# Optimization experiments

Measured on AMD Instinct MI355X. Metric: run time of the kernel, lower is better.

## Reference

```python
import math
import jax, jax.numpy as jnp
import numpy as np

B, N, L, E, H, T = 64, 8, 128, 768, 12, 64


def setup_inputs() -> dict:
    key = jax.random.key(0)
    ks = jax.random.split(key, 8)
    s = 0.02
    return {
        "x":  jax.random.normal(ks[0], (B, N, L, E), dtype=jnp.float32),
        # torch Linear weights are [out, in]
        "Wq": jax.random.normal(ks[1], (H, E, E), dtype=jnp.float32) * s,
        "bq": jax.random.normal(ks[2], (H, E), dtype=jnp.float32) * s,
        "Wv": jax.random.normal(ks[3], (H, T, E), dtype=jnp.float32) * s,
        "bv": jax.random.normal(ks[4], (H, T), dtype=jnp.float32) * s,
        "Wf": jax.random.normal(ks[5], (E, H * T), dtype=jnp.float32) * s,
        "bf": jax.random.normal(ks[6], (E,), dtype=jnp.float32) * s,
    }


def reference(x, Wq, bq, Wv, bv, Wf, bf):
    b, n, l, e = x.shape
    S = b * n                      # set_size after the view(-1, L, E)
    x2 = x.reshape(S, l, e)
    # per-head query projection (batched over heads)
    Q = jnp.einsum('sle,hfe->hslf', x2, Wq) + bq[:, None, None, :]      # [H,S,L,E]
    # raw (unsoftmaxed) attention: (Q K^T) V / sqrt(E)
    scores = jnp.einsum('hslf,smf->hslm', Q, x2)                        # [H,S,L,L]
    attn = jnp.einsum('hslm,sme->hsle', scores, x2) * (1.0 / math.sqrt(e))
    # per-head value projection to transformer_dim
    V = jnp.einsum('hsle,hte->hslt', attn, Wv) + bv[:, None, None, :]   # [H,S,L,T]
    # concat heads along last dim (head order preserved)
    cat = jnp.transpose(V, (1, 2, 0, 3)).reshape(S, l, -1)              # [S,L,H*T]
    out = cat @ Wf.T + bf                                               # [S,L,E]
    return out.reshape(b, n, l, e)
```

## Files before the change

### kernel.cpp

```cpp
#include <hip/hip_runtime.h>
#include <stdint.h>


#define EE 768
#define SLOT 50331648L

typedef short s16x8 __attribute__((ext_vector_type(8)));
typedef float f32x4 __attribute__((ext_vector_type(4)));

__device__ __forceinline__ short f2bf(float f){
  union { float fv; uint32_t u; } v; v.fv = f;
  uint32_t r = (v.u + 0x7fffu + ((v.u >> 16) & 1u)) >> 16;
  return (short)r;
}

__device__ __forceinline__ void gld_lds16(const short* g, short* l){
  __builtin_amdgcn_global_load_lds(
      (const __attribute__((address_space(1))) void*)(uintptr_t)g,
      (__attribute__((address_space(3))) void*)(uintptr_t)l,
      16, 0, 0);
}

__device__ __forceinline__ int xcd_swz(int bid, int nwg){
  int xcd = bid & 7, loc = bid >> 3;
  int q = nwg >> 3, r = nwg & 7;
  return (xcd < r ? xcd * (q + 1) : r * (q + 1) + (xcd - r) * q) + loc;
}

__device__ __forceinline__ int swz64(int row, int c){ return c ^ ((row & 7) << 3); }
__device__ __forceinline__ int swz32(int row, int c){ return c ^ (((row >> 1) & 3) << 3); }

__global__ __launch_bounds__(256) void cast_bf16_k(const float* __restrict__ src,
                                                   short* __restrict__ dst,
                                                   long n, float scale){
  long i = ((long)blockIdx.x * 256 + threadIdx.x) * 8;
  if(i >= n) return;
  float4 a = *(const float4*)(src + i);
  float4 b = *(const float4*)(src + i + 4);
  s16x8 o;
  o[0]=f2bf(a.x*scale); o[1]=f2bf(a.y*scale); o[2]=f2bf(a.z*scale); o[3]=f2bf(a.w*scale);
  o[4]=f2bf(b.x*scale); o[5]=f2bf(b.y*scale); o[6]=f2bf(b.z*scale); o[7]=f2bf(b.w*scale);
  *(s16x8*)(dst + i) = o;
}

__global__ __launch_bounds__(256) void cvec_k(const float* __restrict__ Wf,
                                              const float* __restrict__ bv,
                                              const float* __restrict__ bfv,
                                              float* __restrict__ c){
  int e = blockIdx.x * 256 + threadIdx.x;
  if(e >= EE) return;
  float s = bfv[e];
  for(int k = 0; k < EE; ++k) s += Wf[(long)e * EE + k] * bv[k];
  c[e] = s;
}

__global__ __launch_bounds__(256) void bias_build(const float* __restrict__ bq,
                                                  float* __restrict__ biasQP){
  int i = blockIdx.x * 256 + threadIdx.x;
  if(i < 9984) biasQP[i] = (i < 9216) ? bq[i] : 0.f;
}

template<bool OUTF32>
__global__ __launch_bounds__(512, 1) void gemm8ph(const short* __restrict__ A,
                                                  const short* __restrict__ W,
                                                  const float* __restrict__ bias,
                                                  void* __restrict__ OutBase,
                                                  int hBase, int nSub, int pSub){
  extern __shared__ short lds[];
  const int tid = threadIdx.x, lane = tid & 63, w = tid >> 6;
  const int wr = w >> 2, wc = w & 3;
  const int bid = xcd_swz(blockIdx.x, nSub * 768);
  const int g = bid / 768, rb = bid - g * 768;
  const int rowBlk = rb / 3, colBlk = rb - rowBlk * 3;
  const long rowA0 = (long)rowBlk * 256;
  const int colB0 = colBlk * 256;
  const int wh = (g == pSub) ? 12 : hBase + g;
  const short* Bm = W + (long)wh * 589824L;

  const int slr = w * 16 + (lane >> 2);
  const int scol = swz32(slr, (lane & 3) * 8);
  const short* gA0 = A + (rowA0 + slr) * 768 + scol;
  const short* gA1 = A + (rowA0 + 128 + slr) * 768 + scol;
  const short* gB0 = Bm + (long)(colB0 + slr) * 768 + scol;
  const short* gB1 = Bm + (long)(colB0 + 128 + slr) * 768 + scol;

  auto stageA = [&](int kt){
    short* Al = lds + (kt & 3) * 16384;
    gld_lds16(gA0 + kt * 32, Al + (w * 16) * 32);
    gld_lds16(gA1 + kt * 32, Al + (128 + w * 16) * 32);
  };
  auto stageB = [&](int kt){
    short* Bl = lds + (kt & 3) * 16384 + 8192;
    gld_lds16(gB0 + kt * 32, Bl + (w * 16) * 32);
    gld_lds16(gB1 + kt * 32, Bl + (128 + w * 16) * 32);
  };

  f32x4 acc[8][4] = {};
  const int fr = lane & 15, fc = (lane >> 4) * 8;

  stageA(0); stageB(0); stageA(1); stageB(1); stageA(2); stageB(2);
  asm volatile("s_waitcnt vmcnt(8)\n\ts_barrier" ::: "memory");

  for(int t = 0; t < 24; ++t){
    const short* Al = lds + (t & 3) * 16384;
    const short* Bl = Al + 8192;
    s16x8 bfr[4], af[4];
    #pragma unroll
    for(int n = 0; n < 4; ++n){
      int row = wc * 64 + n * 16 + fr;
      bfr[n] = *(const s16x8*)&Bl[row * 32 + swz32(row, fc)];
    }
    #pragma unroll
    for(int m = 0; m < 4; ++m){
      int row = wr * 128 + m * 16 + fr;
      af[m] = *(const s16x8*)&Al[row * 32 + swz32(row, fc)];
    }
    if(t < 21) stageA(t + 3);
    asm volatile("s_barrier" ::: "memory");
    __builtin_amdgcn_s_setprio(1);
    #pragma unroll
    for(int m = 0; m < 4; ++m)
      #pragma unroll
      for(int n = 0; n < 4; ++n)
        acc[m][n] = __builtin_amdgcn_mfma_f32_16x16x32_bf16(af[m], bfr[n], acc[m][n], 0, 0, 0);
    __builtin_amdgcn_s_setprio(0);
    asm volatile("s_barrier" ::: "memory");
    #pragma unroll
    for(int m = 0; m < 4; ++m){
      int row = wr * 128 + 64 + m * 16 + fr;
      af[m] = *(const s16x8*)&Al[row * 32 + swz32(row, fc)];
    }
    if(t < 21) stageB(t + 3);
    if(t < 21)       asm volatile("s_waitcnt vmcnt(8)" ::: "memory");
    else if(t == 21) asm volatile("s_waitcnt vmcnt(4)" ::: "memory");
    else             asm volatile("s_waitcnt vmcnt(0)" ::: "memory");
    asm volatile("s_barrier" ::: "memory");
    __builtin_amdgcn_s_setprio(1);
    #pragma unroll
    for(int m = 0; m < 4; ++m)
      #pragma unroll
      for(int n = 0; n < 4; ++n)
        acc[4 + m][n] = __builtin_amdgcn_mfma_f32_16x16x32_bf16(af[m], bfr[n], acc[4 + m][n], 0, 0, 0);
    __builtin_amdgcn_s_setprio(0);
    asm volatile("s_barrier" ::: "memory");
  }

  asm volatile("s_waitcnt vmcnt(0) lgkmcnt(0)" ::: "memory");
  __syncthreads();

  float bb[4];
  #pragma unroll
  for(int n = 0; n < 4; ++n)
    bb[n] = bias[wh * 768 + colB0 + wc * 64 + n * 16 + fr];

  if constexpr(!OUTF32){
    short* Out = (short*)OutBase + (long)g * SLOT;
    short* Cs = lds;
    #pragma unroll
    for(int ch = 0; ch < 2; ++ch){
      __syncthreads();
      if(wr == ch){
        #pragma unroll
        for(int m = 0; m < 8; ++m)
          #pragma unroll
          for(int n = 0; n < 4; ++n)
            #pragma unroll
            for(int r2 = 0; r2 < 4; ++r2){
              int row = m * 16 + (lane >> 4) * 4 + r2;
              int c = wc * 64 + n * 16 + fr;
              Cs[row * 256 + (c ^ (((row >> 2) & 3) << 4))] = f2bf(acc[m][n][r2] + bb[n]);
            }
      }
      __syncthreads();
      #pragma unroll
      for(int i = 0; i < 8; ++i){
        int idx = i * 512 + tid;
        int row = idx >> 5, cl = (idx & 31) * 8;
        s16x8 v = *(const s16x8*)&Cs[row * 256 + (cl ^ (((row >> 2) & 3) << 4))];
        *(s16x8*)&Out[(rowA0 + ch * 128 + row) * 768 + colB0 + cl] = v;
      }
    }
  } else {
    float* Co = (float*)OutBase;
    const long crow0 = rowA0 + wr * 128;
    #pragma unroll
    for(int mf = 0; mf < 8; ++mf)
      #pragma unroll
      for(int n = 0; n < 4; ++n)
        #pragma unroll
        for(int r2 = 0; r2 < 4; ++r2){
          const long row = crow0 + mf * 16 + (lane >> 4) * 4 + r2;
          const int col = colB0 + wc * 64 + n * 16 + fr;
          Co[row * 768 + col] = acc[mf][n][r2] + bb[n];
        }
  }
}

__global__ __launch_bounds__(512, 1) void gemm256(const short* __restrict__ A,
                                                  const short* __restrict__ W,
                                                  const float* __restrict__ bias,
                                                  short* __restrict__ OutBase,
                                                  int hBase, int nSub, int pSub){
  __shared__ short lds[2][16384];
  const int tid = threadIdx.x, lane = tid & 63, w = tid >> 6;
  const int wr = w >> 2, wc = w & 3;
  const int bid = xcd_swz(blockIdx.x, nSub * 768);
  const int g = bid / 768, rb = bid - g * 768;
  const int rowBlk = rb / 3, colBlk = rb - rowBlk * 3;
  const long rowA0 = (long)rowBlk * 256;
  const int colB0 = colBlk * 256;
  const int wh = (g == pSub) ? 12 : hBase + g;
  const short* Bm = W + (long)wh * 589824L;
  short* Out = OutBase + (long)g * SLOT;

  const int sr0 = w * 32 + (lane >> 2);
  const int sr1 = sr0 + 16;
  const int scol = (lane & 3) * 8;
  const int sc0 = swz32(sr0, scol);
  const int sc1 = swz32(sr1, scol);
  const short* Ar0 = A + (rowA0 + sr0) * 768;
  const short* Ar1 = A + (rowA0 + sr1) * 768;
  const short* Br0 = Bm + (long)(colB0 + sr0) * 768;
  const short* Br1 = Bm + (long)(colB0 + sr1) * 768;

  f32x4 acc[8][4] = {};
  s16x8 af[4], bf0[2], bf1[2];
  const int fr = lane & 15, fc = (lane >> 4) * 8;

  auto stage = [&](int b, int kt){
    short* Al = &lds[b][0];
    short* Bl = &lds[b][8192];
    gld_lds16(Ar0 + kt + sc0, Al + (w * 2) * 512);
    gld_lds16(Ar1 + kt + sc1, Al + (w * 2 + 1) * 512);
    gld_lds16(Br0 + kt + sc0, Bl + (w * 2) * 512);
    gld_lds16(Br1 + kt + sc1, Bl + (w * 2 + 1) * 512);
  };

  stage(0, 0);
  for(int t = 0; t < 24; ++t){
    if(t < 23){
      stage((t + 1) & 1, (t + 1) * 32);
      asm volatile("s_waitcnt vmcnt(4)\n\ts_barrier" ::: "memory");
    } else {
      asm volatile("s_waitcnt vmcnt(0)\n\ts_barrier" ::: "memory");
    }
    const short* Al = &lds[t & 1][0];
    const short* Bl = &lds[t & 1][8192];

    auto loadA = [&](int mh){
      #pragma unroll
      for(int m = 0; m < 4; ++m){
        int row = wr * 128 + (mh * 4 + m) * 16 + fr;
        af[m] = *(const s16x8*)&Al[row * 32 + swz32(row, fc)];
      }
    };
    auto loadB = [&](int nh, s16x8* bf){
      #pragma unroll
      for(int n = 0; n < 2; ++n){
        int row = wc * 64 + (nh * 2 + n) * 16 + fr;
        bf[n] = *(const s16x8*)&Bl[row * 32 + swz32(row, fc)];
      }
    };
    auto mm = [&](int mh, int nh, s16x8* bf){
      __builtin_amdgcn_s_setprio(1);
      #pragma unroll
      for(int m = 0; m < 4; ++m)
        #pragma unroll
        for(int n = 0; n < 2; ++n)
          acc[mh * 4 + m][nh * 2 + n] = __builtin_amdgcn_mfma_f32_16x16x32_bf16(
              af[m], bf[n], acc[mh * 4 + m][nh * 2 + n], 0, 0, 0);
      __builtin_amdgcn_s_setprio(0);
    };

    loadA(0); loadB(0, bf0); mm(0, 0, bf0);
    loadB(1, bf1);           mm(0, 1, bf1);
    loadA(1);                mm(1, 1, bf1);
    loadB(0, bf0);           mm(1, 0, bf0);
    asm volatile("s_barrier" ::: "memory");
  }

  float bb[4];
  #pragma unroll
  for(int n = 0; n < 4; ++n)
    bb[n] = bias[wh * 768 + colB0 + wc * 64 + n * 16 + fr];

  short* Cs = &lds[0][0];
  #pragma unroll
  for(int ch = 0; ch < 2; ++ch){
    __syncthreads();
    if(wr == ch){
      #pragma unroll
      for(int m = 0; m < 8; ++m)
        #pragma unroll
        for(int n = 0; n < 4; ++n)
          #pragma unroll
          for(int r2 = 0; r2 < 4; ++r2){
            int row = m * 16 + (lane >> 4) * 4 + r2;
            int c = wc * 64 + n * 16 + fr;
            Cs[row * 256 + (c ^ (((row >> 2) & 3) << 4))] = f2bf(acc[m][n][r2] + bb[n]);
          }
    }
    __syncthreads();
    #pragma unroll
    for(int i = 0; i < 8; ++i){
      int idx = i * 512 + tid;
      int row = idx >> 5, cl = (idx & 31) * 8;
      s16x8 v = *(const s16x8*)&Cs[row * 256 + (cl ^ (((row >> 2) & 3) << 4))];
      *(s16x8*)&Out[(rowA0 + ch * 128 + row) * 768 + colB0 + cl] = v;
    }
  }
}

__global__ __launch_bounds__(256, 2) void gemm_f32(const short* __restrict__ A,
                                                   const short* __restrict__ B,
                                                   const float* __restrict__ bias,
                                                   float* __restrict__ Cout){
  __shared__ short smem[4 * 8192];
  const int tid = threadIdx.x, lane = tid & 63, w = tid >> 6;
  const int wr = w >> 1, wc = w & 1;
  const int nCol = 6;
  const int xcd = blockIdx.x & 7, loc = blockIdx.x >> 3;
  const int width = nCol << 3;
  const int gid = loc / width, rem = loc % width;
  const int rowBlk = (xcd << 6) + (gid << 3) + (rem & 7);
  const int colBlk = rem >> 3;
  const long rowA0 = (long)rowBlk << 7;
  const long colB0 = (long)colBlk << 7;
  const int lr = lane >> 3;
  const int sA = swz64(lr, (lane & 7) * 8);

  f32x4 acc[4][4] = {};
  auto stage = [&](int b, int kt){
    short* As = smem + b * 16384;
    #pragma unroll
    for(int it = 0; it < 4; ++it){
      int r = it * 32 + w * 8;
      gld_lds16(&A[(rowA0 + r + lr) * 768 + kt + sA], &As[r * 64]);
      gld_lds16(&B[(colB0 + r + lr) * 768 + kt + sA], &As[8192 + r * 64]);
    }
  };

  stage(0, 0);
  for(int t = 0; t < 12; ++t){
    const int cur = t & 1;
    if(t < 11){
      stage(cur ^ 1, (t + 1) * 64);
      asm volatile("s_waitcnt vmcnt(8)\n\ts_barrier" ::: "memory");
    } else {
      asm volatile("s_waitcnt vmcnt(0)\n\ts_barrier" ::: "memory");
    }
    const short* As = smem + cur * 16384;
    const short* Bs = As + 8192;
    #pragma unroll
    for(int kk = 0; kk < 2; ++kk){
      s16x8 af[4], bfr[4];
      #pragma unroll
      for(int m = 0; m < 4; ++m){
        int row = wr * 64 + m * 16 + (lane & 15);
        af[m] = *(const s16x8*)&As[row * 64 + swz64(row, kk * 32 + (lane >> 4) * 8)];
      }
      #pragma unroll
      for(int n = 0; n < 4; ++n){
        int row = wc * 64 + n * 16 + (lane & 15);
        bfr[n] = *(const s16x8*)&Bs[row * 64 + swz64(row, kk * 32 + (lane >> 4) * 8)];
      }
      #pragma unroll
      for(int m = 0; m < 4; ++m)
        #pragma unroll
        for(int n = 0; n < 4; ++n)
          acc[m][n] = __builtin_amdgcn_mfma_f32_16x16x32_bf16(af[m], bfr[n], acc[m][n], 0, 0, 0);
    }
    asm volatile("s_barrier" ::: "memory");
  }

  const long crow0 = rowA0 + wr * 64;
  const long ccol0 = colB0 + wc * 64;
  #pragma unroll
  for(int n = 0; n < 4; ++n){
    const long col = ccol0 + n * 16 + (lane & 15);
    const float bbv = bias[col];
    #pragma unroll
    for(int m = 0; m < 4; ++m)
      #pragma unroll
      for(int r = 0; r < 4; ++r){
        const long row = crow0 + m * 16 + (lane >> 4) * 4 + r;
        Cout[row * 768 + col] = acc[m][n][r] + bbv;
      }
  }
}

__global__ __launch_bounds__(256, 2) void attn_k(const short* __restrict__ Q,
                                                 const short* __restrict__ P,
                                                 const short* __restrict__ X,
                                                 short* __restrict__ Cat,
                                                 int h0, int nH){
  __shared__ short smem[4 * 8192];
  const int tid = threadIdx.x, lane = tid & 63, w = tid >> 6;
  const int wr = w >> 1, wc = w & 1;
  const int nwg = nH << 9;
  const int bid = xcd_swz(blockIdx.x, nwg);
  const int s = bid / nH, hi = bid - s * nH, h = h0 + hi;
  const long row0 = (long)s * 128;
  const int lr = lane >> 3;
  const int sA = swz64(lr, (lane & 7) * 8);

  const int pm = tid >> 3, pt0 = (tid & 7) * 8;
  s16x8 pv[4];
  #pragma unroll
  for(int i = 0; i < 4; ++i)
    pv[i] = *(const s16x8*)&P[(row0 + pm + i * 32) * 768L + h * 64 + pt0];

  f32x4 acc[4][4] = {};
  const short* Qh = Q + (long)hi * SLOT;
  auto stage = [&](int b, int kt){
    short* As = smem + b * 16384;
    #pragma unroll
    for(int it = 0; it < 4; ++it){
      int r = it * 32 + w * 8;
      gld_lds16(&Qh[(row0 + r + lr) * 768L + kt + sA], &As[r * 64]);
      gld_lds16(&X[(row0 + r + lr) * 768L + kt + sA], &As[8192 + r * 64]);
    }
  };

  stage(0, 0);
  for(int t = 0; t < 12; ++t){
    const int cur = t & 1;
    if(t < 11){
      stage(cur ^ 1, (t + 1) * 64);
      asm volatile("s_waitcnt vmcnt(8)\n\ts_barrier" ::: "memory");
    } else {
      asm volatile("s_waitcnt vmcnt(0)\n\ts_barrier" ::: "memory");
    }
    const short* As = smem + cur * 16384;
    const short* Bs = As + 8192;
    #pragma unroll
    for(int kk = 0; kk < 2; ++kk){
      s16x8 af[4], bfr[4];
      #pragma unroll
      for(int m = 0; m < 4; ++m){
        int row = wr * 64 + m * 16 + (lane & 15);
        af[m] = *(const s16x8*)&As[row * 64 + swz64(row, kk * 32 + (lane >> 4) * 8)];
      }
      #pragma unroll
      for(int n = 0; n < 4; ++n){
        int row = wc * 64 + n * 16 + (lane & 15);
        bfr[n] = *(const s16x8*)&Bs[row * 64 + swz64(row, kk * 32 + (lane >> 4) * 8)];
      }
      #pragma unroll
      for(int m = 0; m < 4; ++m)
        #pragma unroll
        for(int n = 0; n < 4; ++n)
          acc[m][n] = __builtin_amdgcn_mfma_f32_16x16x32_bf16(af[m], bfr[n], acc[m][n], 0, 0, 0);
    }
    asm volatile("s_barrier" ::: "memory");
  }

  short* Pt = smem;
  short* Vt = smem + 8192;
  short* Ss = smem + 16384;

  #pragma unroll
  for(int m = 0; m < 4; ++m)
    #pragma unroll
    for(int n = 0; n < 4; ++n)
      #pragma unroll
      for(int r = 0; r < 4; ++r){
        int row = wr * 64 + m * 16 + (lane >> 4) * 4 + r;
        int c = wc * 64 + n * 16 + (lane & 15);
        Ss[row * 128 + swz64(row, c)] = f2bf(acc[m][n][r]);
      }
  #pragma unroll
  for(int i = 0; i < 4; ++i)
    #pragma unroll
    for(int j = 0; j < 8; ++j){
      int trow = pt0 + j;
      int mc = pm + i * 32;
      Pt[trow * 128 + swz64(trow, mc)] = pv[i][j];
    }
  __syncthreads();

  f32x4 accv[2][4] = {};
  #pragma unroll
  for(int kk = 0; kk < 4; ++kk){
    s16x8 a2[2], b4[4];
    #pragma unroll
    for(int m = 0; m < 2; ++m){
      int row = w * 32 + m * 16 + (lane & 15);
      a2[m] = *(const s16x8*)&Ss[row * 128 + swz64(row, kk * 32 + (lane >> 4) * 8)];
    }
    #pragma unroll
    for(int n = 0; n < 4; ++n){
      int trow = n * 16 + (lane & 15);
      b4[n] = *(const s16x8*)&Pt[trow * 128 + swz64(trow, kk * 32 + (lane >> 4) * 8)];
    }
    #pragma unroll
    for(int m = 0; m < 2; ++m)
      #pragma unroll
      for(int n = 0; n < 4; ++n)
        accv[m][n] = __builtin_amdgcn_mfma_f32_16x16x32_bf16(a2[m], b4[n], accv[m][n], 0, 0, 0);
  }

  #pragma unroll
  for(int m = 0; m < 2; ++m)
    #pragma unroll
    for(int n = 0; n < 4; ++n)
      #pragma unroll
      for(int r = 0; r < 4; ++r){
        int row = w * 32 + m * 16 + (lane >> 4) * 4 + r;
        int c = n * 16 + (lane & 15);
        Vt[row * 64 + swz64(row, c)] = f2bf(accv[m][n][r]);
      }
  __syncthreads();
  #pragma unroll
  for(int k2 = 0; k2 < 4; ++k2){
    int row = k2 * 32 + (tid >> 3);
    int cl = (tid & 7) * 8;
    s16x8 v = *(const s16x8*)&Vt[row * 64 + swz64(row, cl)];
    *(s16x8*)&Cat[(row0 + row) * 768L + h * 64 + cl] = v;
  }
}

extern "C" void kernel_launch(void* const* d_in, const int* in_sizes, int n_in,
                              void* d_out, int out_size, void* d_ws, size_t ws_size,
                              hipStream_t stream){
  const float* x  = (const float*)d_in[0];
  const float* Wq = (const float*)d_in[1];
  const float* bq = (const float*)d_in[2];
  const float* Wv = (const float*)d_in[3];
  const float* bv = (const float*)d_in[4];
  const float* Wf = (const float*)d_in[5];
  const float* bfv= (const float*)d_in[6];

  const float rsqE = 0.03608439182435161f;
  char* ws = (char*)d_ws;

  short* Xb  = (short*)(ws);
  short* Cat = (short*)(ws + 100663296L);
  short* Wb  = (short*)(ws + 201326592L);
  short* Wfb = (short*)(ws + 216662016L);
  float* bQP = (float*)(ws + 217841664L);
  float* cv  = (float*)(ws + 217881600L);
  short* QS  = (short*)(ws + 217884672L);

  const size_t QOFF = 217884672ULL;
  int G = 1;
  const int cands[5] = {12, 6, 4, 3, 2};
  for(int i = 0; i < 5; ++i)
    if(ws_size >= QOFF + (size_t)(cands[i] + 1) * 100663296ULL){ G = cands[i]; break; }
  short* Pall = QS + (long)G * SLOT;

  bool deep =
      hipFuncSetAttribute(reinterpret_cast<const void*>(&gemm8ph<false>),
                          hipFuncAttributeMaxDynamicSharedMemorySize, 131072) == hipSuccess &&
      hipFuncSetAttribute(reinterpret_cast<const void*>(&gemm8ph<true>),
                          hipFuncAttributeMaxDynamicSharedMemorySize, 131072) == hipSuccess;

  dim3 b256(256), b512(512);
  cast_bf16_k<<<24576, b256, 0, stream>>>(x,  Xb, 50331648L, 1.f);
  cast_bf16_k<<<3456,  b256, 0, stream>>>(Wq, Wb, 7077888L, 1.f);
  cast_bf16_k<<<288,   b256, 0, stream>>>(Wv, Wb + 7077888L, 589824L, rsqE);
  cast_bf16_k<<<288,   b256, 0, stream>>>(Wf, Wfb, 589824L, 1.f);
  bias_build<<<39, b256, 0, stream>>>(bq, bQP);
  cvec_k<<<3, b256, 0, stream>>>(Wf, bv, bfv, cv);

  const int nB = 12 / G;
  for(int b = 0; b < nB; ++b){
    const int nSub = G + (b == 0 ? 1 : 0);
    const int pSub = (b == 0) ? G : -1;
    if(deep)
      gemm8ph<false><<<dim3(nSub * 768), b512, 131072, stream>>>(Xb, Wb, bQP, QS, b * G, nSub, pSub);
    else
      gemm256<<<dim3(nSub * 768), b512, 0, stream>>>(Xb, Wb, bQP, QS, b * G, nSub, pSub);
    attn_k<<<dim3(G * 512), b256, 0, stream>>>(QS, Pall, Xb, Cat, b * G, G);
  }
  if(deep)
    gemm8ph<true><<<dim3(768), b512, 131072, stream>>>(Cat, Wfb, cv, d_out, 0, 1, -1);
  else
    gemm_f32<<<dim3(3072), b256, 0, stream>>>(Cat, Wfb, cv, (float*)d_out);
}
```

Measured before the change: 1.765 ms.

## Rewrite GEMM main loop with register double-buffered fragments and fused staging

The projection GEMM's main loop drops the eight-phase schedule, which split the A fragments into two halves with four barriers per k-step. Each k-step now issues one combined A+B async load into the LDS ring and takes a single barrier. Fragments for the next k-tile are read into a second register set while MFMAs run on the current one. This cuts barrier count and lets LDS reads overlap with matrix math, at the cost of more VGPRs and a possible write-after-read race on the LDS ring, since slots are refilled without a barrier after the last read.

```diff
diff --git a/kernel.cpp b/kernel.cpp
--- a/kernel.cpp
+++ b/kernel.cpp
@@ -61,7 +61,7 @@
 }
 
 template<bool OUTF32>
-__global__ __launch_bounds__(512, 1) void gemm8ph(const short* __restrict__ A,
+__global__ __launch_bounds__(512, 1) void gemm_rb(const short* __restrict__ A,
                                                   const short* __restrict__ W,
                                                   const float* __restrict__ bias,
                                                   void* __restrict__ OutBase,
@@ -84,66 +84,74 @@
   const short* gB0 = Bm + (long)(colB0 + slr) * 768 + scol;
   const short* gB1 = Bm + (long)(colB0 + 128 + slr) * 768 + scol;
 
-  auto stageA = [&](int kt){
+  auto stageK = [&](int kt){
     short* Al = lds + (kt & 3) * 16384;
     gld_lds16(gA0 + kt * 32, Al + (w * 16) * 32);
     gld_lds16(gA1 + kt * 32, Al + (128 + w * 16) * 32);
-  };
-  auto stageB = [&](int kt){
-    short* Bl = lds + (kt & 3) * 16384 + 8192;
-    gld_lds16(gB0 + kt * 32, Bl + (w * 16) * 32);
-    gld_lds16(gB1 + kt * 32, Bl + (128 + w * 16) * 32);
+    gld_lds16(gB0 + kt * 32, Al + 8192 + (w * 16) * 32);
+    gld_lds16(gB1 + kt * 32, Al + 8192 + (128 + w * 16) * 32);
   };
 
   f32x4 acc[8][4] = {};
   const int fr = lane & 15, fc = (lane >> 4) * 8;
 
-  stageA(0); stageB(0); stageA(1); stageB(1); stageA(2); stageB(2);
-  asm volatile("s_waitcnt vmcnt(8)\n\ts_barrier" ::: "memory");
-
-  for(int t = 0; t < 24; ++t){
+  s16x8 A0[8], B0[4], A1[8], B1[4];
+
+  auto readF = [&](int t, s16x8* Af, s16x8* Bf){
     const short* Al = lds + (t & 3) * 16384;
     const short* Bl = Al + 8192;
-    s16x8 bfr[4], af[4];
+    #pragma unroll
+    for(int m = 0; m < 8; ++m){
+      int row = wr * 128 + m * 16 + fr;
+      Af[m] = *(const s16x8*)&Al[row * 32 + swz32(row, fc)];
+    }
     #pragma unroll
     for(int n = 0; n < 4; ++n){
       int row = wc * 64 + n * 16 + fr;
-      bfr[n] = *(const s16x8*)&Bl[row * 32 + swz32(row, fc)];
-    }
-    #pragma unroll
-    for(int m = 0; m < 4; ++m){
-      int row = wr * 128 + m * 16 + fr;
-      af[m] = *(const s16x8*)&Al[row * 32 + swz32(row, fc)];
-    }
-    if(t < 21) stageA(t + 3);
-    asm volatile("s_barrier" ::: "memory");
+      Bf[n] = *(const s16x8*)&Bl[row * 32 + swz32(row, fc)];
+    }
+  };
+  auto mfmaC = [&](s16x8* Af, s16x8* Bf){
     __builtin_amdgcn_s_setprio(1);
     #pragma unroll
-    for(int m = 0; m < 4; ++m)
+    for(int m = 0; m < 8; ++m)
       #pragma unroll
       for(int n = 0; n < 4; ++n)
-        acc[m][n] = __builtin_amdgcn_mfma_f32_16x16x32_bf16(af[m], bfr[n], acc[m][n], 0, 0, 0);
+        acc[m][n] = __builtin_amdgcn_mfma_f32_16x16x32_bf16(Af[m], Bf[n], acc[m][n], 0, 0, 0);
     __builtin_amdgcn_s_setprio(0);
-    asm volatile("s_barrier" ::: "memory");
-    #pragma unroll
-    for(int m = 0; m < 4; ++m){
-      int row = wr * 128 + 64 + m * 16 + fr;
-      af[m] = *(const s16x8*)&Al[row * 32 + swz32(row, fc)];
-    }
-    if(t < 21) stageB(t + 3);
-    if(t < 21)       asm volatile("s_waitcnt vmcnt(8)" ::: "memory");
-    else if(t == 21) asm volatile("s_waitcnt vmcnt(4)" ::: "memory");
-    else             asm volatile("s_waitcnt vmcnt(0)" ::: "memory");
-    asm volatile("s_barrier" ::: "memory");
-    __builtin_amdgcn_s_setprio(1);
-    #pragma unroll
-    for(int m = 0; m < 4; ++m)
-      #pragma unroll
-      for(int n = 0; n < 4; ++n)
-        acc[4 + m][n] = __builtin_amdgcn_mfma_f32_16x16x32_bf16(af[m], bfr[n], acc[4 + m][n], 0, 0, 0);
-    __builtin_amdgcn_s_setprio(0);
-    asm volatile("s_barrier" ::: "memory");
-  }
+  };
+
+  stageK(0); stageK(1); stageK(2);
+  asm volatile("s_waitcnt vmcnt(8)" ::: "memory");
+  __builtin_amdgcn_s_barrier();
+  readF(0, A0, B0);
+
+  for(int tt = 0; tt < 20; tt += 2){
+    stageK(tt + 3);
+    asm volatile("s_waitcnt vmcnt(8)" ::: "memory");
+    __builtin_amdgcn_s_barrier();
+    readF(tt + 1, A1, B1);
+    mfmaC(A0, B0);
+    stageK(tt + 4);
+    asm volatile("s_waitcnt vmcnt(8)" ::: "memory");
+    __builtin_amdgcn_s_barrier();
+    readF(tt + 2, A0, B0);
+    mfmaC(A1, B1);
+  }
+  stageK(23);
+  asm volatile("s_waitcnt vmcnt(8)" ::: "memory");
+  __builtin_amdgcn_s_barrier();
+  readF(21, A1, B1);
+  mfmaC(A0, B0);
+  asm volatile("s_waitcnt vmcnt(4)" ::: "memory");
+  __builtin_amdgcn_s_barrier();
+  readF(22, A0, B0);
+  mfmaC(A1, B1);
+  asm volatile("s_waitcnt vmcnt(0)" ::: "memory");
+  __builtin_amdgcn_s_barrier();
+  readF(23, A1, B1);
+  mfmaC(A0, B0);
+  mfmaC(A1, B1);
 
   asm volatile("s_waitcnt vmcnt(0) lgkmcnt(0)" ::: "memory");
   __syncthreads();
@@ -550,9 +558,9 @@
   short* Pall = QS + (long)G * SLOT;
 
   bool deep =
-      hipFuncSetAttribute(reinterpret_cast<const void*>(&gemm8ph<false>),
+      hipFuncSetAttribute(reinterpret_cast<const void*>(&gemm_rb<false>),
                           hipFuncAttributeMaxDynamicSharedMemorySize, 131072) == hipSuccess &&
-      hipFuncSetAttribute(reinterpret_cast<const void*>(&gemm8ph<true>),
+      hipFuncSetAttribute(reinterpret_cast<const void*>(&gemm_rb<true>),
                           hipFuncAttributeMaxDynamicSharedMemorySize, 131072) == hipSuccess;
 
   dim3 b256(256), b512(512);
@@ -568,13 +576,13 @@
     const int nSub = G + (b == 0 ? 1 : 0);
     const int pSub = (b == 0) ? G : -1;
     if(deep)
-      gemm8ph<false><<<dim3(nSub * 768), b512, 131072, stream>>>(Xb, Wb, bQP, QS, b * G, nSub, pSub);
+      gemm_rb<false><<<dim3(nSub * 768), b512, 131072, stream>>>(Xb, Wb, bQP, QS, b * G, nSub, pSub);
     else
       gemm256<<<dim3(nSub * 768), b512, 0, stream>>>(Xb, Wb, bQP, QS, b * G, nSub, pSub);
     attn_k<<<dim3(G * 512), b256, 0, stream>>>(QS, Pall, Xb, Cat, b * G, G);
   }
   if(deep)
-    gemm8ph<true><<<dim3(768), b512, 131072, stream>>>(Cat, Wfb, cv, d_out, 0, 1, -1);
+    gemm_rb<true><<<dim3(768), b512, 131072, stream>>>(Cat, Wfb, cv, d_out, 0, 1, -1);
   else
     gemm_f32<<<dim3(3072), b256, 0, stream>>>(Cat, Wfb, cv, (float*)d_out);
 }
```

Result: no change. 1.769 ms (+0.2%).

## Switch GEMM to 32x32x16 MFMA tiles with unified A/B staging

Applied to the files above, without the earlier changes.

Replaces the 16x16x32 bf16 MFMA tiling in the main GEMM kernel with 32x32x16 MFMAs, which gives each wave 4x2 accumulator tiles and halves the LDS fragment reads per FLOP. A and B stages for each k-tile are now issued together instead of being split across two phases, and both k-halves are read from LDS up front. The epilogue index mapping is rewritten for the 32x32 accumulator layout. Risks include a different LDS bank-conflict pattern under the existing swizzle, higher register pressure, and changed overlap of loads with compute.

```diff
diff --git a/kernel.cpp b/kernel.cpp
--- a/kernel.cpp
+++ b/kernel.cpp
@@ -7,6 +7,7 @@
 
 typedef short s16x8 __attribute__((ext_vector_type(8)));
 typedef float f32x4 __attribute__((ext_vector_type(4)));
+typedef float f32x16 __attribute__((ext_vector_type(16)));
 
 __device__ __forceinline__ short f2bf(float f){
   union { float fv; uint32_t u; } v; v.fv = f;
@@ -61,11 +62,11 @@
 }
 
 template<bool OUTF32>
-__global__ __launch_bounds__(512, 1) void gemm8ph(const short* __restrict__ A,
-                                                  const short* __restrict__ W,
-                                                  const float* __restrict__ bias,
-                                                  void* __restrict__ OutBase,
-                                                  int hBase, int nSub, int pSub){
+__global__ __launch_bounds__(512, 1) void gemm32(const short* __restrict__ A,
+                                                 const short* __restrict__ W,
+                                                 const float* __restrict__ bias,
+                                                 void* __restrict__ OutBase,
+                                                 int hBase, int nSub, int pSub){
   extern __shared__ short lds[];
   const int tid = threadIdx.x, lane = tid & 63, w = tid >> 6;
   const int wr = w >> 2, wc = w & 3;
@@ -84,74 +85,70 @@
   const short* gB0 = Bm + (long)(colB0 + slr) * 768 + scol;
   const short* gB1 = Bm + (long)(colB0 + 128 + slr) * 768 + scol;
 
-  auto stageA = [&](int kt){
+  auto stageK = [&](int kt){
     short* Al = lds + (kt & 3) * 16384;
     gld_lds16(gA0 + kt * 32, Al + (w * 16) * 32);
     gld_lds16(gA1 + kt * 32, Al + (128 + w * 16) * 32);
+    gld_lds16(gB0 + kt * 32, Al + 8192 + (w * 16) * 32);
+    gld_lds16(gB1 + kt * 32, Al + 8192 + (128 + w * 16) * 32);
   };
-  auto stageB = [&](int kt){
-    short* Bl = lds + (kt & 3) * 16384 + 8192;
-    gld_lds16(gB0 + kt * 32, Bl + (w * 16) * 32);
-    gld_lds16(gB1 + kt * 32, Bl + (128 + w * 16) * 32);
-  };
-
-  f32x4 acc[8][4] = {};
-  const int fr = lane & 15, fc = (lane >> 4) * 8;
-
-  stageA(0); stageB(0); stageA(1); stageB(1); stageA(2); stageB(2);
-  asm volatile("s_waitcnt vmcnt(8)\n\ts_barrier" ::: "memory");
-
-  for(int t = 0; t < 24; ++t){
+
+  f32x16 acc[4][2] = {};
+  const int lrow = lane & 31;
+  const int kh = (lane >> 5) * 8;
+
+  auto readAB = [&](int t, int kk, s16x8* Af, s16x8* Bf){
     const short* Al = lds + (t & 3) * 16384;
     const short* Bl = Al + 8192;
-    s16x8 bfr[4], af[4];
-    #pragma unroll
-    for(int n = 0; n < 4; ++n){
-      int row = wc * 64 + n * 16 + fr;
-      bfr[n] = *(const s16x8*)&Bl[row * 32 + swz32(row, fc)];
-    }
-    #pragma unroll
-    for(int m = 0; m < 4; ++m){
-      int row = wr * 128 + m * 16 + fr;
-      af[m] = *(const s16x8*)&Al[row * 32 + swz32(row, fc)];
-    }
-    if(t < 21) stageA(t + 3);
-    asm volatile("s_barrier" ::: "memory");
+    const int colv = kk * 16 + kh;
+    #pragma unroll
+    for(int rt = 0; rt < 4; ++rt){
+      int row = wr * 128 + rt * 32 + lrow;
+      Af[rt] = *(const s16x8*)&Al[row * 32 + swz32(row, colv)];
+    }
+    #pragma unroll
+    for(int ct = 0; ct < 2; ++ct){
+      int row = wc * 64 + ct * 32 + lrow;
+      Bf[ct] = *(const s16x8*)&Bl[row * 32 + swz32(row, colv)];
+    }
+  };
+  auto mm8 = [&](s16x8* Af, s16x8* Bf){
     __builtin_amdgcn_s_setprio(1);
     #pragma unroll
-    for(int m = 0; m < 4; ++m)
-      #pragma unroll
-      for(int n = 0; n < 4; ++n)
-        acc[m][n] = __builtin_amdgcn_mfma_f32_16x16x32_bf16(af[m], bfr[n], acc[m][n], 0, 0, 0);
+    for(int rt = 0; rt < 4; ++rt)
+      #pragma unroll
+      for(int ct = 0; ct < 2; ++ct)
+        acc[rt][ct] = __builtin_amdgcn_mfma_f32_32x32x16_bf16(Af[rt], Bf[ct], acc[rt][ct], 0, 0, 0);
     __builtin_amdgcn_s_setprio(0);
-    asm volatile("s_barrier" ::: "memory");
-    #pragma unroll
-    for(int m = 0; m < 4; ++m){
-      int row = wr * 128 + 64 + m * 16 + fr;
-      af[m] = *(const s16x8*)&Al[row * 32 + swz32(row, fc)];
-    }
-    if(t < 21) stageB(t + 3);
+  };
+
+  stageK(0); stageK(1); stageK(2);
+  asm volatile("s_waitcnt vmcnt(8)" ::: "memory");
+  asm volatile("s_barrier" ::: "memory");
+
+  for(int t = 0; t < 24; ++t){
+    s16x8 Af0[4], Bf0[2], Af1[4], Bf1[2];
+    readAB(t, 0, Af0, Bf0);
+    readAB(t, 1, Af1, Bf1);
+    if(t < 21) stageK(t + 3);
+    mm8(Af0, Bf0);
     if(t < 21)       asm volatile("s_waitcnt vmcnt(8)" ::: "memory");
     else if(t == 21) asm volatile("s_waitcnt vmcnt(4)" ::: "memory");
-    else             asm volatile("s_waitcnt vmcnt(0)" ::: "memory");
+    else if(t == 22) asm volatile("s_waitcnt vmcnt(0)" ::: "memory");
     asm volatile("s_barrier" ::: "memory");
-    __builtin_amdgcn_s_setprio(1);
-    #pragma unroll
-    for(int m = 0; m < 4; ++m)
-      #pragma unroll
-      for(int n = 0; n < 4; ++n)
-        acc[4 + m][n] = __builtin_amdgcn_mfma_f32_16x16x32_bf16(af[m], bfr[n], acc[4 + m][n], 0, 0, 0);
-    __builtin_amdgcn_s_setprio(0);
+    mm8(Af1, Bf1);
     asm volatile("s_barrier" ::: "memory");
   }
 
   asm volatile("s_waitcnt vmcnt(0) lgkmcnt(0)" ::: "memory");
   __syncthreads();
 
-  float bb[4];
-  #pragma unroll
-  for(int n = 0; n < 4; ++n)
-    bb[n] = bias[wh * 768 + colB0 + wc * 64 + n * 16 + fr];
+  float bb[2];
+  #pragma unroll
+  for(int ct = 0; ct < 2; ++ct)
+    bb[ct] = bias[wh * 768 + colB0 + wc * 64 + ct * 32 + lrow];
+
+  const int rbase = (lane >> 5) * 4;
 
   if constexpr(!OUTF32){
     short* Out = (short*)OutBase + (long)g * SLOT;
@@ -161,14 +158,14 @@
       __syncthreads();
       if(wr == ch){
         #pragma unroll
-        for(int m = 0; m < 8; ++m)
+        for(int rt = 0; rt < 4; ++rt)
           #pragma unroll
-          for(int n = 0; n < 4; ++n)
+          for(int ct = 0; ct < 2; ++ct)
             #pragma unroll
-            for(int r2 = 0; r2 < 4; ++r2){
-              int row = m * 16 + (lane >> 4) * 4 + r2;
-              int c = wc * 64 + n * 16 + fr;
-              Cs[row * 256 + (c ^ (((row >> 2) & 3) << 4))] = f2bf(acc[m][n][r2] + bb[n]);
+            for(int reg = 0; reg < 16; ++reg){
+              int row = rt * 32 + rbase + (reg & 3) + 8 * (reg >> 2);
+              int c = wc * 64 + ct * 32 + lrow;
+              Cs[row * 256 + (c ^ (((row >> 2) & 3) << 4))] = f2bf(acc[rt][ct][reg] + bb[ct]);
             }
       }
       __syncthreads();
@@ -182,16 +179,15 @@
     }
   } else {
     float* Co = (float*)OutBase;
-    const long crow0 = rowA0 + wr * 128;
-    #pragma unroll
-    for(int mf = 0; mf < 8; ++mf)
-      #pragma unroll
-      for(int n = 0; n < 4; ++n)
+    #pragma unroll
+    for(int rt = 0; rt < 4; ++rt)
+      #pragma unroll
+      for(int ct = 0; ct < 2; ++ct)
         #pragma unroll
-        for(int r2 = 0; r2 < 4; ++r2){
-          const long row = crow0 + mf * 16 + (lane >> 4) * 4 + r2;
-          const int col = colB0 + wc * 64 + n * 16 + fr;
-          Co[row * 768 + col] = acc[mf][n][r2] + bb[n];
+        for(int reg = 0; reg < 16; ++reg){
+          long row = rowA0 + wr * 128 + rt * 32 + rbase + (reg & 3) + 8 * (reg >> 2);
+          int col = colB0 + wc * 64 + ct * 32 + lrow;
+          Co[row * 768 + col] = acc[rt][ct][reg] + bb[ct];
         }
   }
 }
@@ -550,9 +546,9 @@
   short* Pall = QS + (long)G * SLOT;
 
   bool deep =
-      hipFuncSetAttribute(reinterpret_cast<const void*>(&gemm8ph<false>),
+      hipFuncSetAttribute(reinterpret_cast<const void*>(&gemm32<false>),
                           hipFuncAttributeMaxDynamicSharedMemorySize, 131072) == hipSuccess &&
-      hipFuncSetAttribute(reinterpret_cast<const void*>(&gemm8ph<true>),
+      hipFuncSetAttribute(reinterpret_cast<const void*>(&gemm32<true>),
                           hipFuncAttributeMaxDynamicSharedMemorySize, 131072) == hipSuccess;
 
   dim3 b256(256), b512(512);
@@ -568,13 +564,13 @@
     const int nSub = G + (b == 0 ? 1 : 0);
     const int pSub = (b == 0) ? G : -1;
     if(deep)
-      gemm8ph<false><<<dim3(nSub * 768), b512, 131072, stream>>>(Xb, Wb, bQP, QS, b * G, nSub, pSub);
+      gemm32<false><<<dim3(nSub * 768), b512, 131072, stream>>>(Xb, Wb, bQP, QS, b * G, nSub, pSub);
     else
       gemm256<<<dim3(nSub * 768), b512, 0, stream>>>(Xb, Wb, bQP, QS, b * G, nSub, pSub);
     attn_k<<<dim3(G * 512), b256, 0, stream>>>(QS, Pall, Xb, Cat, b * G, G);
   }
   if(deep)
-    gemm8ph<true><<<dim3(768), b512, 131072, stream>>>(Cat, Wfb, cv, d_out, 0, 1, -1);
+    gemm32<true><<<dim3(768), b512, 131072, stream>>>(Cat, Wfb, cv, d_out, 0, 1, -1);
   else
     gemm_f32<<<dim3(3072), b256, 0, stream>>>(Cat, Wfb, cv, (float*)d_out);
 }
```

Result: slower. 1.846 ms (+4.6%).

## Replace 4-stage BK32 GEMM pipeline with double-buffered BK64 kernel

Applied to the files above, without the earlier changes.

The deep-LDS projection GEMM goes from a 4-deep ring of 32-wide K tiles with interleaved A/B staging and split MFMA phases to a simple double-buffered scheme with 64-wide K tiles. That means 12 iterations, one barrier per tile and a 64-column swizzle. The intent is fewer barriers and waitcnts per unit of MFMA work and larger global_load_lds batches. The cost is shallower prefetch, so load latency may be less well hidden. The final output projection no longer uses the fp32 variant of the deep kernel and always runs the existing gemm_f32 path.

```diff
diff --git a/kernel.cpp b/kernel.cpp
--- a/kernel.cpp
+++ b/kernel.cpp
@@ -60,12 +60,11 @@
   if(i < 9984) biasQP[i] = (i < 9216) ? bq[i] : 0.f;
 }
 
-template<bool OUTF32>
-__global__ __launch_bounds__(512, 1) void gemm8ph(const short* __restrict__ A,
-                                                  const short* __restrict__ W,
-                                                  const float* __restrict__ bias,
-                                                  void* __restrict__ OutBase,
-                                                  int hBase, int nSub, int pSub){
+__global__ __launch_bounds__(512, 1) void gemm64(const short* __restrict__ A,
+                                                 const short* __restrict__ W,
+                                                 const float* __restrict__ bias,
+                                                 short* __restrict__ OutBase,
+                                                 int hBase, int nSub, int pSub){
   extern __shared__ short lds[];
   const int tid = threadIdx.x, lane = tid & 63, w = tid >> 6;
   const int wr = w >> 2, wc = w & 3;
@@ -77,71 +76,57 @@
   const int wh = (g == pSub) ? 12 : hBase + g;
   const short* Bm = W + (long)wh * 589824L;
 
-  const int slr = w * 16 + (lane >> 2);
-  const int scol = swz32(slr, (lane & 3) * 8);
-  const short* gA0 = A + (rowA0 + slr) * 768 + scol;
-  const short* gA1 = A + (rowA0 + 128 + slr) * 768 + scol;
-  const short* gB0 = Bm + (long)(colB0 + slr) * 768 + scol;
-  const short* gB1 = Bm + (long)(colB0 + 128 + slr) * 768 + scol;
-
-  auto stageA = [&](int kt){
-    short* Al = lds + (kt & 3) * 16384;
-    gld_lds16(gA0 + kt * 32, Al + (w * 16) * 32);
-    gld_lds16(gA1 + kt * 32, Al + (128 + w * 16) * 32);
+  const int srow = tid >> 3;
+  const int ssw = swz64(srow, (tid & 7) * 8);
+  const short* gA = A + (rowA0 + srow) * 768 + ssw;
+  const short* gB = Bm + (long)(colB0 + srow) * 768 + ssw;
+
+  auto stage = [&](int b, int kt){
+    short* Al = lds + b * 32768;
+    short* Bl = Al + 16384;
+    #pragma unroll
+    for(int j = 0; j < 4; ++j){
+      gld_lds16(gA + (long)j * 49152 + kt, Al + j * 4096 + w * 512);
+      gld_lds16(gB + (long)j * 49152 + kt, Bl + j * 4096 + w * 512);
+    }
   };
-  auto stageB = [&](int kt){
-    short* Bl = lds + (kt & 3) * 16384 + 8192;
-    gld_lds16(gB0 + kt * 32, Bl + (w * 16) * 32);
-    gld_lds16(gB1 + kt * 32, Bl + (128 + w * 16) * 32);
-  };
 
   f32x4 acc[8][4] = {};
-  const int fr = lane & 15, fc = (lane >> 4) * 8;
-
-  stageA(0); stageB(0); stageA(1); stageB(1); stageA(2); stageB(2);
-  asm volatile("s_waitcnt vmcnt(8)\n\ts_barrier" ::: "memory");
-
-  for(int t = 0; t < 24; ++t){
-    const short* Al = lds + (t & 3) * 16384;
-    const short* Bl = Al + 8192;
-    s16x8 bfr[4], af[4];
-    #pragma unroll
-    for(int n = 0; n < 4; ++n){
-      int row = wc * 64 + n * 16 + fr;
-      bfr[n] = *(const s16x8*)&Bl[row * 32 + swz32(row, fc)];
-    }
-    #pragma unroll
-    for(int m = 0; m < 4; ++m){
-      int row = wr * 128 + m * 16 + fr;
-      af[m] = *(const s16x8*)&Al[row * 32 + swz32(row, fc)];
-    }
-    if(t < 21) stageA(t + 3);
-    asm volatile("s_barrier" ::: "memory");
-    __builtin_amdgcn_s_setprio(1);
-    #pragma unroll
-    for(int m = 0; m < 4; ++m)
-      #pragma unroll
-      for(int n = 0; n < 4; ++n)
-        acc[m][n] = __builtin_amdgcn_mfma_f32_16x16x32_bf16(af[m], bfr[n], acc[m][n], 0, 0, 0);
-    __builtin_amdgcn_s_setprio(0);
-    asm volatile("s_barrier" ::: "memory");
-    #pragma unroll
-    for(int m = 0; m < 4; ++m){
-      int row = wr * 128 + 64 + m * 16 + fr;
-      af[m] = *(const s16x8*)&Al[row * 32 + swz32(row, fc)];
-    }
-    if(t < 21) stageB(t + 3);
-    if(t < 21)       asm volatile("s_waitcnt vmcnt(8)" ::: "memory");
-    else if(t == 21) asm volatile("s_waitcnt vmcnt(4)" ::: "memory");
-    else             asm volatile("s_waitcnt vmcnt(0)" ::: "memory");
-    asm volatile("s_barrier" ::: "memory");
-    __builtin_amdgcn_s_setprio(1);
-    #pragma unroll
-    for(int m = 0; m < 4; ++m)
-      #pragma unroll
-      for(int n = 0; n < 4; ++n)
-        acc[4 + m][n] = __builtin_amdgcn_mfma_f32_16x16x32_bf16(af[m], bfr[n], acc[4 + m][n], 0, 0, 0);
-    __builtin_amdgcn_s_setprio(0);
+  const int fr = lane & 15, fcb = (lane >> 4) * 8;
+
+  stage(0, 0);
+  for(int t = 0; t < 12; ++t){
+    if(t < 11){
+      stage((t + 1) & 1, (t + 1) * 64);
+      asm volatile("s_waitcnt vmcnt(8)\n\ts_barrier" ::: "memory");
+    } else {
+      asm volatile("s_waitcnt vmcnt(0)\n\ts_barrier" ::: "memory");
+    }
+    const short* Al = lds + (t & 1) * 32768;
+    const short* Bl = Al + 16384;
+
+    #pragma unroll
+    for(int kk = 0; kk < 2; ++kk){
+      s16x8 af[8], bf[4];
+      const int colv = kk * 32 + fcb;
+      #pragma unroll
+      for(int m = 0; m < 8; ++m){
+        int row = wr * 128 + m * 16 + fr;
+        af[m] = *(const s16x8*)&Al[row * 64 + swz64(row, colv)];
+      }
+      #pragma unroll
+      for(int n = 0; n < 4; ++n){
+        int row = wc * 64 + n * 16 + fr;
+        bf[n] = *(const s16x8*)&Bl[row * 64 + swz64(row, colv)];
+      }
+      __builtin_amdgcn_s_setprio(1);
+      #pragma unroll
+      for(int m = 0; m < 8; ++m)
+        #pragma unroll
+        for(int n = 0; n < 4; ++n)
+          acc[m][n] = __builtin_amdgcn_mfma_f32_16x16x32_bf16(af[m], bf[n], acc[m][n], 0, 0, 0);
+      __builtin_amdgcn_s_setprio(0);
+    }
     asm volatile("s_barrier" ::: "memory");
   }
 
@@ -153,46 +138,31 @@
   for(int n = 0; n < 4; ++n)
     bb[n] = bias[wh * 768 + colB0 + wc * 64 + n * 16 + fr];
 
-  if constexpr(!OUTF32){
-    short* Out = (short*)OutBase + (long)g * SLOT;
-    short* Cs = lds;
-    #pragma unroll
-    for(int ch = 0; ch < 2; ++ch){
-      __syncthreads();
-      if(wr == ch){
+  short* Out = OutBase + (long)g * SLOT;
+  short* Cs = lds;
+  #pragma unroll
+  for(int ch = 0; ch < 2; ++ch){
+    __syncthreads();
+    if(wr == ch){
+      #pragma unroll
+      for(int m = 0; m < 8; ++m)
         #pragma unroll
-        for(int m = 0; m < 8; ++m)
+        for(int n = 0; n < 4; ++n)
           #pragma unroll
-          for(int n = 0; n < 4; ++n)
-            #pragma unroll
-            for(int r2 = 0; r2 < 4; ++r2){
-              int row = m * 16 + (lane >> 4) * 4 + r2;
-              int c = wc * 64 + n * 16 + fr;
-              Cs[row * 256 + (c ^ (((row >> 2) & 3) << 4))] = f2bf(acc[m][n][r2] + bb[n]);
-            }
-      }
-      __syncthreads();
-      #pragma unroll
-      for(int i = 0; i < 8; ++i){
-        int idx = i * 512 + tid;
-        int row = idx >> 5, cl = (idx & 31) * 8;
-        s16x8 v = *(const s16x8*)&Cs[row * 256 + (cl ^ (((row >> 2) & 3) << 4))];
-        *(s16x8*)&Out[(rowA0 + ch * 128 + row) * 768 + colB0 + cl] = v;
-      }
-    }
-  } else {
-    float* Co = (float*)OutBase;
-    const long crow0 = rowA0 + wr * 128;
-    #pragma unroll
-    for(int mf = 0; mf < 8; ++mf)
-      #pragma unroll
-      for(int n = 0; n < 4; ++n)
-        #pragma unroll
-        for(int r2 = 0; r2 < 4; ++r2){
-          const long row = crow0 + mf * 16 + (lane >> 4) * 4 + r2;
-          const int col = colB0 + wc * 64 + n * 16 + fr;
-          Co[row * 768 + col] = acc[mf][n][r2] + bb[n];
-        }
+          for(int r2 = 0; r2 < 4; ++r2){
+            int row = m * 16 + (lane >> 4) * 4 + r2;
+            int c = wc * 64 + n * 16 + fr;
+            Cs[row * 256 + (c ^ (((row >> 2) & 3) << 4))] = f2bf(acc[m][n][r2] + bb[n]);
+          }
+    }
+    __syncthreads();
+    #pragma unroll
+    for(int i = 0; i < 8; ++i){
+      int idx = i * 512 + tid;
+      int row = idx >> 5, cl = (idx & 31) * 8;
+      s16x8 v = *(const s16x8*)&Cs[row * 256 + (cl ^ (((row >> 2) & 3) << 4))];
+      *(s16x8*)&Out[(rowA0 + ch * 128 + row) * 768 + colB0 + cl] = v;
+    }
   }
 }
 
@@ -549,11 +519,8 @@
     if(ws_size >= QOFF + (size_t)(cands[i] + 1) * 100663296ULL){ G = cands[i]; break; }
   short* Pall = QS + (long)G * SLOT;
 
-  bool deep =
-      hipFuncSetAttribute(reinterpret_cast<const void*>(&gemm8ph<false>),
-                          hipFuncAttributeMaxDynamicSharedMemorySize, 131072) == hipSuccess &&
-      hipFuncSetAttribute(reinterpret_cast<const void*>(&gemm8ph<true>),
-                          hipFuncAttributeMaxDynamicSharedMemorySize, 131072) == hipSuccess;
+  bool deep = hipFuncSetAttribute(reinterpret_cast<const void*>(&gemm64),
+                  hipFuncAttributeMaxDynamicSharedMemorySize, 131072) == hipSuccess;
 
   dim3 b256(256), b512(512);
   cast_bf16_k<<<24576, b256, 0, stream>>>(x,  Xb, 50331648L, 1.f);
@@ -568,13 +535,10 @@
     const int nSub = G + (b == 0 ? 1 : 0);
     const int pSub = (b == 0) ? G : -1;
     if(deep)
-      gemm8ph<false><<<dim3(nSub * 768), b512, 131072, stream>>>(Xb, Wb, bQP, QS, b * G, nSub, pSub);
+      gemm64<<<dim3(nSub * 768), b512, 131072, stream>>>(Xb, Wb, bQP, QS, b * G, nSub, pSub);
     else
       gemm256<<<dim3(nSub * 768), b512, 0, stream>>>(Xb, Wb, bQP, QS, b * G, nSub, pSub);
     attn_k<<<dim3(G * 512), b256, 0, stream>>>(QS, Pall, Xb, Cat, b * G, G);
   }
-  if(deep)
-    gemm8ph<true><<<dim3(768), b512, 131072, stream>>>(Cat, Wfb, cv, d_out, 0, 1, -1);
-  else
-    gemm_f32<<<dim3(3072), b256, 0, stream>>>(Cat, Wfb, cv, (float*)d_out);
-}
+  gemm_f32<<<dim3(3072), b256, 0, stream>>>(Cat, Wfb, cv, (float*)d_out);
+}
```

Result: no change. 1.743 ms (-1.3%).
